# Optimization experiments

Hardware: AMD Instinct MI355X
Metric: run time of the kernel (lower is better)

## Reference

```python
import jax, jax.numpy as jnp
import numpy as np

M, K, N = 4096, 4096, 11008

def setup_inputs() -> dict:
    key = jax.random.key(0)
    k1, k2, k3, k4, k5 = jax.random.split(key, 5)
    x = jax.random.normal(k1, (M, K), dtype=jnp.float32)
    # int8 weights stored as int32 carrier (values in [-128, 127])
    weight = jax.random.randint(k2, (N, K), -128, 128, dtype=jnp.int32)
    # per-channel dequant scale, small positive values
    deq_scale = jax.random.uniform(k3, (N,), dtype=jnp.float32, minval=1e-4, maxval=2e-3)
    # static per-tensor activation scale
    input_scale = jax.random.uniform(k4, (1,), dtype=jnp.float32, minval=0.02, maxval=0.05)
    input_offset = jnp.zeros((1,), dtype=jnp.int32)
    quant_bias = jax.random.randint(k5, (N,), -1000, 1000, dtype=jnp.int32)
    return {"x": x, "weight": weight, "deq_scale": deq_scale,
            "input_scale": input_scale, "input_offset": input_offset,
            "quant_bias": quant_bias}

def reference(x, weight, deq_scale, input_scale, input_offset, quant_bias):
    # Static per-tensor activation quantization to int8
    x_q = jnp.clip(jnp.round(x / input_scale) + input_offset.astype(jnp.float32),
                   -128.0, 127.0).astype(jnp.int32)  # [M, K]
    # int8 GEMM accumulated in int32 (weight stored [N, K], i.e. transposed)
    acc = jnp.einsum('mk,nk->mn', x_q, weight)  # [M, N] int32
    # add int32 quant bias, per-channel dequant to fp32
    out = (acc + quant_bias[None, :]).astype(jnp.float32) * deq_scale[None, :]
    return out
```

## Files before the change

kernel.cpp:

```cpp
#include <hip/hip_runtime.h>
#include <cstdint>
#include <cstddef>

#define M_DIM 4096
#define K_DIM 4096
#define N_DIM 11008
#define BM 256
#define BN 256
#define BKB 128
#define NT (K_DIM / BKB)
#define NITER (NT / 2)
#define NTM (M_DIM / BM)
#define NTN (N_DIM / BN)
#define SLOT_BYTES 65536
#define B_OFF 32768

typedef int   int4v   __attribute__((ext_vector_type(4)));
typedef float float4v __attribute__((ext_vector_type(4)));

__device__ __forceinline__ void gload_lds16(const void* g, void* l) {
  __builtin_amdgcn_global_load_lds(
      (const __attribute__((address_space(1))) unsigned int*)g,
      (__attribute__((address_space(3))) unsigned int*)l, 16, 0, 0);
}

__global__ void quant_x_kernel(const float* __restrict__ x,
                               const float* __restrict__ scale_p,
                               const int* __restrict__ off_p,
                               signed char* __restrict__ xq, int total16) {
  const float inv = 1.0f / scale_p[0];
  const float off = (float)off_p[0];
  int tid = blockIdx.x * blockDim.x + threadIdx.x;
  int stride = gridDim.x * blockDim.x;
  const float4v* x4 = (const float4v*)x;
  int4v* out4 = (int4v*)xq;
  for (int i = tid; i < total16; i += stride) {
    int4v o;
#pragma unroll
    for (int j = 0; j < 4; ++j) {
      float4v v = x4[(size_t)i * 4 + j];
      int r = 0;
#pragma unroll
      for (int e = 0; e < 4; ++e) {
        float q = rintf(v[e] * inv) + off;
        q = fminf(fmaxf(q, -128.0f), 127.0f);
        int qi = (int)q;
        r |= (qi & 0xff) << (8 * e);
      }
      o[j] = r;
    }
    out4[i] = o;
  }
}

__global__ void pack_w_kernel(const int* __restrict__ w,
                              signed char* __restrict__ wq, int total16) {
  int tid = blockIdx.x * blockDim.x + threadIdx.x;
  int stride = gridDim.x * blockDim.x;
  const int4v* w4 = (const int4v*)w;
  int4v* out4 = (int4v*)wq;
  for (int i = tid; i < total16; i += stride) {
    int4v o;
#pragma unroll
    for (int j = 0; j < 4; ++j) {
      int4v v = w4[(size_t)i * 4 + j];
      o[j] = (v[0] & 0xff) | ((v[1] & 0xff) << 8) |
             ((v[2] & 0xff) << 16) | ((v[3] & 0xff) << 24);
    }
    out4[i] = o;
  }
}

__global__ __launch_bounds__(512, 2) void gemm_i8_kernel(
    const signed char* __restrict__ A,
    const signed char* __restrict__ B,
    const int* __restrict__ qbias,
    const float* __restrict__ dscale,
    float* __restrict__ out) {
  __shared__ __attribute__((aligned(16))) signed char lds[2 * SLOT_BYTES];

  const int tid  = threadIdx.x;
  const int lane = tid & 63;
  const int wv   = tid >> 6;
  const int wr   = wv >> 2;
  const int wc   = wv & 3;

  int bid = blockIdx.x;
  int swz = (bid & 7) * 86 + (bid >> 3);
  int tm = swz / NTN;
  int tn = swz % NTN;

  const int sks = wv & 1;
  const int r2  = wv >> 1;
  const int ro  = (r2 & 1) | ((r2 & 2) << 2);

  const signed char* pA = A + (size_t)(tm * BM + ro * 16 + (lane & 15)) * K_DIM
                            + sks * 64 + (lane >> 4) * 16;
  const signed char* pB = B + (size_t)(tn * BN + ro * 16 + (lane & 15)) * K_DIM
                            + sks * 64 + (lane >> 4) * 16;
  const int ldsA0 = (ro * 2 + sks) * 1024;
  const int ldsB0 = B_OFF + (ro * 2 + sks) * 1024;

#define STG(ktS, c) do {                                                      \
    int ktw_ = (ktS) & (NT - 1);                                              \
    int sl_  = (ktw_ & 1) * SLOT_BYTES;                                       \
    gload_lds16(pA + (size_t)(c) * 32 * K_DIM + (size_t)ktw_ * BKB,           \
                lds + sl_ + ldsA0 + (c) * 4096);                              \
    gload_lds16(pB + (size_t)(c) * 32 * K_DIM + (size_t)ktw_ * BKB,           \
                lds + sl_ + ldsB0 + (c) * 4096); } while (0)

  const int rdA0 = (wr * 8) * 2048 + lane * 16;
  const int rdB0 = B_OFF + (wc * 4) * 2048 + lane * 16;

  int4v acc[8][4];
#pragma unroll
  for (int i = 0; i < 8; ++i)
#pragma unroll
    for (int j = 0; j < 4; ++j) acc[i][j] = (int4v){0, 0, 0, 0};

  int4v bfr[4][2], afr[2][2];

#define PHASE(S, P, KTS, CH) do {                                             \
    const int sb_ = (S) * SLOT_BYTES;                                         \
    if ((P) == 0) {                                                           \
      _Pragma("unroll") for (int ni = 0; ni < 4; ++ni)                        \
        _Pragma("unroll") for (int ks = 0; ks < 2; ++ks)                      \
          bfr[ni][ks] = *(const int4v*)(lds + sb_ + rdB0 + ni * 2048 + ks * 1024); \
    }                                                                         \
    _Pragma("unroll") for (int d = 0; d < 2; ++d)                             \
      _Pragma("unroll") for (int ks = 0; ks < 2; ++ks)                        \
        afr[d][ks] = *(const int4v*)(lds + sb_ + rdA0 + (2 * (P) + d) * 2048 + ks * 1024); \
    STG(KTS, CH);                                                             \
    __builtin_amdgcn_s_barrier();                                             \
    asm volatile("s_waitcnt lgkmcnt(0)" ::: "memory");                        \
    __builtin_amdgcn_s_setprio(1);                                            \
    _Pragma("unroll") for (int d = 0; d < 2; ++d)                             \
      _Pragma("unroll") for (int ni = 0; ni < 4; ++ni)                        \
        _Pragma("unroll") for (int ks = 0; ks < 2; ++ks)                      \
          acc[2 * (P) + d][ni] = __builtin_amdgcn_mfma_i32_16x16x64_i8(       \
              afr[d][ks], bfr[ni][ks], acc[2 * (P) + d][ni], 0, 0, 0);        \
    __builtin_amdgcn_s_setprio(0);                                            \
    if ((P) == 3) asm volatile("s_waitcnt vmcnt(6)" ::: "memory");            \
    __builtin_amdgcn_s_barrier();                                             \
  } while (0)

#pragma unroll
  for (int c = 0; c < 4; ++c) STG(0, c);
#pragma unroll
  for (int c = 0; c < 3; ++c) STG(1, c);
  asm volatile("s_waitcnt vmcnt(6)" ::: "memory");
  __builtin_amdgcn_s_barrier();

  for (int t = 0; t < NITER; ++t) {
    const int k0 = 2 * t;
    PHASE(0, 0, k0 + 1, 3);
    PHASE(0, 1, k0 + 2, 0);
    PHASE(0, 2, k0 + 2, 1);
    PHASE(0, 3, k0 + 2, 2);
    PHASE(1, 0, k0 + 2, 3);
    PHASE(1, 1, k0 + 3, 0);
    PHASE(1, 2, k0 + 3, 1);
    PHASE(1, 3, k0 + 3, 2);
  }
  asm volatile("s_waitcnt vmcnt(0)" ::: "memory");
#undef PHASE
#undef STG

  const int col = lane & 15;
  const int rb  = (lane >> 4) * 4;
  const int gm0 = tm * BM + wr * 128;
  const int gn0 = tn * BN + wc * 64;
#pragma unroll
  for (int ni = 0; ni < 4; ++ni) {
    int gn = gn0 + ni * 16 + col;
    float ds = dscale[gn];
    int qb = qbias[gn];
#pragma unroll
    for (int mi = 0; mi < 8; ++mi) {
      int gm = gm0 + mi * 16 + rb;
#pragma unroll
      for (int j = 0; j < 4; ++j)
        out[(size_t)(gm + j) * N_DIM + gn] = (float)(acc[mi][ni][j] + qb) * ds;
    }
  }
}

extern "C" void kernel_launch(void* const* d_in, const int* in_sizes, int n_in,
                              void* d_out, int out_size, void* d_ws, size_t ws_size,
                              hipStream_t stream) {
  const float* x      = (const float*)d_in[0];
  const int*   w      = (const int*)d_in[1];
  const float* dscale = (const float*)d_in[2];
  const float* iscale = (const float*)d_in[3];
  const int*   ioff   = (const int*)d_in[4];
  const int*   qbias  = (const int*)d_in[5];
  float* out = (float*)d_out;

  const size_t xq_bytes = (size_t)M_DIM * K_DIM;
  const size_t wq_bytes = (size_t)N_DIM * K_DIM;
  if (ws_size < xq_bytes + wq_bytes) return;

  signed char* xq = (signed char*)d_ws;
  signed char* wq = (signed char*)d_ws + xq_bytes;

  quant_x_kernel<<<2048, 256, 0, stream>>>(x, iscale, ioff, xq, M_DIM * K_DIM / 16);
  pack_w_kernel<<<2048, 256, 0, stream>>>(w, wq, N_DIM * K_DIM / 16);
  gemm_i8_kernel<<<NTM * NTN, 512, 0, stream>>>(xq, wq, qbias, dscale, out);
}
```

Baseline: 287.0 us.

## Double-buffer register fragments to overlap LDS reads with MFMA in int8 GEMM

Restructures the main loop so LDS fragment reads for the next quarter-tile (and the next k-tile's B fragments) are issued before the MFMAs of the current quarter, using ping-pong A/B register buffers and partial lgkmcnt waits. This removes the full lgkmcnt(0) stall before each MFMA group. It also reduces barriers from two per phase to one and changes the global prefetch depth and vmcnt placement. The cost is higher register pressure, which may spill under launch_bounds(512,2), and a trickier cross-slot synchronization that could race if the waits are miscounted.

```diff
diff --git a/kernel.cpp b/kernel.cpp
--- a/kernel.cpp
+++ b/kernel.cpp
@@ -112,58 +112,94 @@
   const int rdA0 = (wr * 8) * 2048 + lane * 16;
   const int rdB0 = B_OFF + (wc * 4) * 2048 + lane * 16;
 
-  int4v acc[8][4];
-#pragma unroll
-  for (int i = 0; i < 8; ++i)
-#pragma unroll
-    for (int j = 0; j < 4; ++j) acc[i][j] = (int4v){0, 0, 0, 0};
-
-  int4v bfr[4][2], afr[2][2];
-
-#define PHASE(S, P, KTS, CH) do {                                             \
-    const int sb_ = (S) * SLOT_BYTES;                                         \
-    if ((P) == 0) {                                                           \
-      _Pragma("unroll") for (int ni = 0; ni < 4; ++ni)                        \
-        _Pragma("unroll") for (int ks = 0; ks < 2; ++ks)                      \
-          bfr[ni][ks] = *(const int4v*)(lds + sb_ + rdB0 + ni * 2048 + ks * 1024); \
-    }                                                                         \
+#define RD_A(dst, SB, QQ) do {                                                \
     _Pragma("unroll") for (int d = 0; d < 2; ++d)                             \
       _Pragma("unroll") for (int ks = 0; ks < 2; ++ks)                        \
-        afr[d][ks] = *(const int4v*)(lds + sb_ + rdA0 + (2 * (P) + d) * 2048 + ks * 1024); \
-    STG(KTS, CH);                                                             \
-    __builtin_amdgcn_s_barrier();                                             \
-    asm volatile("s_waitcnt lgkmcnt(0)" ::: "memory");                        \
+        dst[d][ks] = *(const int4v*)(lds + (SB) + rdA0 + (2*(QQ)+d)*2048 + ks*1024); \
+  } while (0)
+#define RD_B2(dst, SB, NI0) do {                                              \
+    _Pragma("unroll") for (int ii = 0; ii < 2; ++ii)                          \
+      _Pragma("unroll") for (int ks = 0; ks < 2; ++ks)                        \
+        dst[(NI0)+ii][ks] = *(const int4v*)(lds + (SB) + rdB0 + ((NI0)+ii)*2048 + ks*1024); \
+  } while (0)
+#define MFMA_Q(af, bf, QQ) do {                                               \
     __builtin_amdgcn_s_setprio(1);                                            \
     _Pragma("unroll") for (int d = 0; d < 2; ++d)                             \
       _Pragma("unroll") for (int ni = 0; ni < 4; ++ni)                        \
         _Pragma("unroll") for (int ks = 0; ks < 2; ++ks)                      \
-          acc[2 * (P) + d][ni] = __builtin_amdgcn_mfma_i32_16x16x64_i8(       \
-              afr[d][ks], bfr[ni][ks], acc[2 * (P) + d][ni], 0, 0, 0);        \
+          acc[2*(QQ)+d][ni] = __builtin_amdgcn_mfma_i32_16x16x64_i8(          \
+              af[d][ks], bf[ni][ks], acc[2*(QQ)+d][ni], 0, 0, 0);             \
     __builtin_amdgcn_s_setprio(0);                                            \
-    if ((P) == 3) asm volatile("s_waitcnt vmcnt(6)" ::: "memory");            \
-    __builtin_amdgcn_s_barrier();                                             \
-  } while (0)
+  } while (0)
+#define WAIT_LGKM(n) do {                                                     \
+    asm volatile("s_waitcnt lgkmcnt(" #n ")" ::: "memory");                   \
+    __builtin_amdgcn_sched_barrier(0);                                        \
+  } while (0)
+
+  int4v acc[8][4];
+#pragma unroll
+  for (int i = 0; i < 8; ++i)
+#pragma unroll
+    for (int j = 0; j < 4; ++j) acc[i][j] = (int4v){0, 0, 0, 0};
+
+  int4v afr0[2][2], afr1[2][2], bfr0[4][2], bfr1[4][2];
 
 #pragma unroll
   for (int c = 0; c < 4; ++c) STG(0, c);
 #pragma unroll
-  for (int c = 0; c < 3; ++c) STG(1, c);
-  asm volatile("s_waitcnt vmcnt(6)" ::: "memory");
+  for (int c = 0; c < 4; ++c) STG(1, c);
+  asm volatile("s_waitcnt vmcnt(8)" ::: "memory");
   __builtin_amdgcn_s_barrier();
+  RD_A(afr0, 0, 0);
+  RD_B2(bfr0, 0, 0);
+  RD_B2(bfr0, 0, 2);
+  asm volatile("s_waitcnt lgkmcnt(0)" ::: "memory");
+  __builtin_amdgcn_sched_barrier(0);
+  __builtin_amdgcn_s_barrier();
+
+#define TILE4(S, BFC, BFN, KST) do {                                          \
+    const int SB_  = (S) * SLOT_BYTES;                                        \
+    const int SBn_ = (1 - (S)) * SLOT_BYTES;                                  \
+                                                                      \
+    RD_A(afr1, SB_, 1);                                                       \
+    STG((KST), 0);                                                            \
+    __builtin_amdgcn_s_barrier();                                             \
+    WAIT_LGKM(4);                                                             \
+    MFMA_Q(afr0, BFC, 0);                                                     \
+                                                                      \
+    RD_A(afr0, SB_, 2);                                                       \
+    STG((KST), 1);                                                            \
+    asm volatile("s_waitcnt vmcnt(4)" ::: "memory");     \
+    __builtin_amdgcn_s_barrier();                                             \
+    WAIT_LGKM(4);                                                             \
+    MFMA_Q(afr1, BFC, 1);                                                     \
+                                                                      \
+    RD_A(afr1, SB_, 3);                                                       \
+    RD_B2(BFN, SBn_, 0);                                                      \
+    STG((KST), 2);                                                            \
+    __builtin_amdgcn_s_barrier();                                             \
+    WAIT_LGKM(8);                                                             \
+    MFMA_Q(afr0, BFC, 2);                                                     \
+                                                                      \
+    RD_A(afr0, SBn_, 0);                                                      \
+    RD_B2(BFN, SBn_, 2);                                                      \
+    STG((KST), 3);                                                            \
+    __builtin_amdgcn_s_barrier();                                             \
+    WAIT_LGKM(8);                                                             \
+    MFMA_Q(afr1, BFC, 3);                                                     \
+  } while (0)
 
   for (int t = 0; t < NITER; ++t) {
     const int k0 = 2 * t;
-    PHASE(0, 0, k0 + 1, 3);
-    PHASE(0, 1, k0 + 2, 0);
-    PHASE(0, 2, k0 + 2, 1);
-    PHASE(0, 3, k0 + 2, 2);
-    PHASE(1, 0, k0 + 2, 3);
-    PHASE(1, 1, k0 + 3, 0);
-    PHASE(1, 2, k0 + 3, 1);
-    PHASE(1, 3, k0 + 3, 2);
-  }
-  asm volatile("s_waitcnt vmcnt(0)" ::: "memory");
-#undef PHASE
+    TILE4(0, bfr0, bfr1, k0 + 2);
+    TILE4(1, bfr1, bfr0, k0 + 3);
+  }
+  asm volatile("s_waitcnt vmcnt(0) lgkmcnt(0)" ::: "memory");
+#undef TILE4
+#undef WAIT_LGKM
+#undef MFMA_Q
+#undef RD_B2
+#undef RD_A
 #undef STG
 
   const int col = lane & 15;
```

After: 284.5 us. No clear change (-0.9%).

## Restructure int8 GEMM to 4 waves with 128x128 per-wave tiles and register double-buffering

Applied to the files above, without the earlier changes.

Changes the GEMM block from 8 waves (each holding a 128x64 output tile) to 4 waves that each own a 128x128 tile, so every LDS fragment read feeds more MFMAs. The main loop now double-buffers A/B fragments in registers across the two k-halves and issues the next tile's global-to-LDS loads after a single barrier per k-step. The fine-grained phase schedule is removed, and the block-to-tile swizzle changes. The larger accumulator footprint (64 int4 accumulators plus four 8-entry fragment buffers) raises register pressure and lowers waves per CU, which may cost latency hiding.

```diff
diff --git a/kernel.cpp b/kernel.cpp
--- a/kernel.cpp
+++ b/kernel.cpp
@@ -9,7 +9,6 @@
 #define BN 256
 #define BKB 128
 #define NT (K_DIM / BKB)
-#define NITER (NT / 2)
 #define NTM (M_DIM / BM)
 #define NTN (N_DIM / BN)
 #define SLOT_BYTES 65536
@@ -71,7 +70,7 @@
   }
 }
 
-__global__ __launch_bounds__(512, 2) void gemm_i8_kernel(
+__global__ __launch_bounds__(256, 1) void gemm_i8_kernel(
     const signed char* __restrict__ A,
     const signed char* __restrict__ B,
     const int* __restrict__ qbias,
@@ -82,105 +81,102 @@
   const int tid  = threadIdx.x;
   const int lane = tid & 63;
   const int wv   = tid >> 6;
-  const int wr   = wv >> 2;
-  const int wc   = wv & 3;
+  const int wr   = wv >> 1;
+  const int wc   = wv & 1;
 
   int bid = blockIdx.x;
-  int swz = (bid & 7) * 86 + (bid >> 3);
-  int tm = swz / NTN;
-  int tn = swz % NTN;
-
-  const int sks = wv & 1;
-  const int r2  = wv >> 1;
-  const int ro  = (r2 & 1) | ((r2 & 2) << 2);
-
-  const signed char* pA = A + (size_t)(tm * BM + ro * 16 + (lane & 15)) * K_DIM
-                            + sks * 64 + (lane >> 4) * 16;
-  const signed char* pB = B + (size_t)(tn * BN + ro * 16 + (lane & 15)) * K_DIM
-                            + sks * 64 + (lane >> 4) * 16;
-  const int ldsA0 = (ro * 2 + sks) * 1024;
-  const int ldsB0 = B_OFF + (ro * 2 + sks) * 1024;
-
-#define STG(ktS, c) do {                                                      \
-    int ktw_ = (ktS) & (NT - 1);                                              \
-    int sl_  = (ktw_ & 1) * SLOT_BYTES;                                       \
-    gload_lds16(pA + (size_t)(c) * 32 * K_DIM + (size_t)ktw_ * BKB,           \
-                lds + sl_ + ldsA0 + (c) * 4096);                              \
-    gload_lds16(pB + (size_t)(c) * 32 * K_DIM + (size_t)ktw_ * BKB,           \
-                lds + sl_ + ldsB0 + (c) * 4096); } while (0)
-
-  const int rdA0 = (wr * 8) * 2048 + lane * 16;
-  const int rdB0 = B_OFF + (wc * 4) * 2048 + lane * 16;
-
-  int4v acc[8][4];
+  int s   = bid >> 3;
+  int tm  = 2 * (bid & 7) + (s & 1);
+  int tn  = s >> 1;
+
+  const signed char* pA = A + (size_t)(tm * BM + wv * 64 + (lane & 15)) * K_DIM
+                            + (lane >> 4) * 16;
+  const signed char* pB = B + (size_t)(tn * BN + wv * 64 + (lane & 15)) * K_DIM
+                            + (lane >> 4) * 16;
+
+#define STG(kt, so) do {                                                      \
+    _Pragma("unroll") for (int c = 0; c < 4; ++c)                             \
+      _Pragma("unroll") for (int ks = 0; ks < 2; ++ks) {                      \
+        gload_lds16(pA + (size_t)c * 16 * K_DIM + (size_t)(kt) * BKB + ks * 64, \
+                    lds + (so) + ((((wv * 4 + c) * 2 + ks)) << 10));          \
+        gload_lds16(pB + (size_t)c * 16 * K_DIM + (size_t)(kt) * BKB + ks * 64, \
+                    lds + (so) + B_OFF + ((((wv * 4 + c) * 2 + ks)) << 10));  \
+      } } while (0)
+
+#define RD_A(buf, so, ks) do {                                                \
+    _Pragma("unroll") for (int m = 0; m < 8; ++m)                             \
+      buf[m] = *(const int4v*)(lds + (so) +                                   \
+                (((wr * 8 + m) * 2 + (ks)) << 10) + lane * 16); } while (0)
+#define RD_B(buf, so, ks) do {                                                \
+    _Pragma("unroll") for (int n = 0; n < 8; ++n)                             \
+      buf[n] = *(const int4v*)(lds + (so) + B_OFF +                           \
+                (((wc * 8 + n) * 2 + (ks)) << 10) + lane * 16); } while (0)
+#define MFMA_S(ab, bb) do {                                                   \
+    _Pragma("unroll") for (int m = 0; m < 8; ++m)                             \
+      _Pragma("unroll") for (int n = 0; n < 8; ++n)                           \
+        acc[m][n] = __builtin_amdgcn_mfma_i32_16x16x64_i8(                    \
+            ab[m], bb[n], acc[m][n], 0, 0, 0); } while (0)
+#define WAIT_LGKM(k) do {                                                     \
+    asm volatile("s_waitcnt lgkmcnt(" #k ")" ::: "memory");                   \
+    __builtin_amdgcn_sched_barrier(0); } while (0)
+
+  int4v acc[8][8];
 #pragma unroll
   for (int i = 0; i < 8; ++i)
 #pragma unroll
-    for (int j = 0; j < 4; ++j) acc[i][j] = (int4v){0, 0, 0, 0};
-
-  int4v bfr[4][2], afr[2][2];
-
-#define PHASE(S, P, KTS, CH) do {                                             \
-    const int sb_ = (S) * SLOT_BYTES;                                         \
-    if ((P) == 0) {                                                           \
-      _Pragma("unroll") for (int ni = 0; ni < 4; ++ni)                        \
-        _Pragma("unroll") for (int ks = 0; ks < 2; ++ks)                      \
-          bfr[ni][ks] = *(const int4v*)(lds + sb_ + rdB0 + ni * 2048 + ks * 1024); \
-    }                                                                         \
-    _Pragma("unroll") for (int d = 0; d < 2; ++d)                             \
-      _Pragma("unroll") for (int ks = 0; ks < 2; ++ks)                        \
-        afr[d][ks] = *(const int4v*)(lds + sb_ + rdA0 + (2 * (P) + d) * 2048 + ks * 1024); \
-    STG(KTS, CH);                                                             \
-    __builtin_amdgcn_s_barrier();                                             \
-    asm volatile("s_waitcnt lgkmcnt(0)" ::: "memory");                        \
-    __builtin_amdgcn_s_setprio(1);                                            \
-    _Pragma("unroll") for (int d = 0; d < 2; ++d)                             \
-      _Pragma("unroll") for (int ni = 0; ni < 4; ++ni)                        \
-        _Pragma("unroll") for (int ks = 0; ks < 2; ++ks)                      \
-          acc[2 * (P) + d][ni] = __builtin_amdgcn_mfma_i32_16x16x64_i8(       \
-              afr[d][ks], bfr[ni][ks], acc[2 * (P) + d][ni], 0, 0, 0);        \
-    __builtin_amdgcn_s_setprio(0);                                            \
-    if ((P) == 3) asm volatile("s_waitcnt vmcnt(6)" ::: "memory");            \
-    __builtin_amdgcn_s_barrier();                                             \
-  } while (0)
-
-#pragma unroll
-  for (int c = 0; c < 4; ++c) STG(0, c);
-#pragma unroll
-  for (int c = 0; c < 3; ++c) STG(1, c);
-  asm volatile("s_waitcnt vmcnt(6)" ::: "memory");
+    for (int j = 0; j < 8; ++j) acc[i][j] = (int4v){0, 0, 0, 0};
+
+  int4v A0[8], A1[8], B0[8], B1[8];
+
+  STG(0, 0);
+  STG(1, SLOT_BYTES);
+  asm volatile("s_waitcnt vmcnt(16)" ::: "memory");
   __builtin_amdgcn_s_barrier();
-
-  for (int t = 0; t < NITER; ++t) {
-    const int k0 = 2 * t;
-    PHASE(0, 0, k0 + 1, 3);
-    PHASE(0, 1, k0 + 2, 0);
-    PHASE(0, 2, k0 + 2, 1);
-    PHASE(0, 3, k0 + 2, 2);
-    PHASE(1, 0, k0 + 2, 3);
-    PHASE(1, 1, k0 + 3, 0);
-    PHASE(1, 2, k0 + 3, 1);
-    PHASE(1, 3, k0 + 3, 2);
-  }
-  asm volatile("s_waitcnt vmcnt(0)" ::: "memory");
-#undef PHASE
+  __builtin_amdgcn_sched_barrier(0);
+  RD_A(A0, 0, 0);
+  RD_B(B0, 0, 0);
+
+  for (int kt = 0; kt < NT; ++kt) {
+    const int cur = (kt & 1) * SLOT_BYTES;
+    const int nxt = cur ^ SLOT_BYTES;
+
+    RD_A(A1, cur, 1);
+    WAIT_LGKM(8);
+    RD_B(B1, cur, 1);
+    MFMA_S(A0, B0);
+    WAIT_LGKM(8);
+    asm volatile("s_waitcnt vmcnt(0)" ::: "memory");
+    WAIT_LGKM(0);
+    __builtin_amdgcn_s_barrier();
+    __builtin_amdgcn_sched_barrier(0);
+    if (kt + 2 < NT) STG(kt + 2, cur);
+    if (kt + 1 < NT) {
+      RD_A(A0, nxt, 0);
+      RD_B(B0, nxt, 0);
+    }
+    MFMA_S(A1, B1);
+  }
+#undef WAIT_LGKM
+#undef MFMA_S
+#undef RD_B
+#undef RD_A
 #undef STG
 
   const int col = lane & 15;
   const int rb  = (lane >> 4) * 4;
   const int gm0 = tm * BM + wr * 128;
-  const int gn0 = tn * BN + wc * 64;
-#pragma unroll
-  for (int ni = 0; ni < 4; ++ni) {
-    int gn = gn0 + ni * 16 + col;
+  const int gn0 = tn * BN + wc * 128;
+#pragma unroll
+  for (int n = 0; n < 8; ++n) {
+    int gn = gn0 + n * 16 + col;
     float ds = dscale[gn];
     int qb = qbias[gn];
 #pragma unroll
-    for (int mi = 0; mi < 8; ++mi) {
-      int gm = gm0 + mi * 16 + rb;
+    for (int m = 0; m < 8; ++m) {
+      int gm = gm0 + m * 16 + rb;
 #pragma unroll
       for (int j = 0; j < 4; ++j)
-        out[(size_t)(gm + j) * N_DIM + gn] = (float)(acc[mi][ni][j] + qb) * ds;
+        out[(size_t)(gm + j) * N_DIM + gn] = (float)(acc[m][n][j] + qb) * ds;
     }
   }
 }
@@ -205,5 +201,5 @@
 
   quant_x_kernel<<<2048, 256, 0, stream>>>(x, iscale, ioff, xq, M_DIM * K_DIM / 16);
   pack_w_kernel<<<2048, 256, 0, stream>>>(w, wq, N_DIM * K_DIM / 16);
-  gemm_i8_kernel<<<NTM * NTN, 512, 0, stream>>>(xq, wq, qbias, dscale, out);
-}
+  gemm_i8_kernel<<<NTM * NTN, 256, 0, stream>>>(xq, wq, qbias, dscale, out);
+}
```

Measured after the change: 365.1 us. +27.2%, slower.

## Use XOR-swizzled LDS layout for int8 GEMM tiles and remap block order

Applied to the files above, without the earlier changes.

Changes the global-to-LDS staging so each row of A and B is stored contiguously with an XOR column swizzle. Reads use matching swizzled offsets, which should cut LDS bank conflicts on fragment loads. It also changes the block-to-tile mapping so consecutive blocks share B tiles across pairs of M tiles, and restructures the main loop into four phases per K step with alternating A fragment buffers. Barrier and waitcnt placement are reworked, which risks ordering hazards or added synchronisation cost.

```diff
diff --git a/kernel.cpp b/kernel.cpp
--- a/kernel.cpp
+++ b/kernel.cpp
@@ -9,7 +9,6 @@
 #define BN 256
 #define BKB 128
 #define NT (K_DIM / BKB)
-#define NITER (NT / 2)
 #define NTM (M_DIM / BM)
 #define NTN (N_DIM / BN)
 #define SLOT_BYTES 65536
@@ -86,85 +85,99 @@
   const int wc   = wv & 3;
 
   int bid = blockIdx.x;
-  int swz = (bid & 7) * 86 + (bid >> 3);
-  int tm = swz / NTN;
-  int tn = swz % NTN;
-
-  const int sks = wv & 1;
-  const int r2  = wv >> 1;
-  const int ro  = (r2 & 1) | ((r2 & 2) << 2);
-
-  const signed char* pA = A + (size_t)(tm * BM + ro * 16 + (lane & 15)) * K_DIM
-                            + sks * 64 + (lane >> 4) * 16;
-  const signed char* pB = B + (size_t)(tn * BN + ro * 16 + (lane & 15)) * K_DIM
-                            + sks * 64 + (lane >> 4) * 16;
-  const int ldsA0 = (ro * 2 + sks) * 1024;
-  const int ldsB0 = B_OFF + (ro * 2 + sks) * 1024;
-
-#define STG(ktS, c) do {                                                      \
-    int ktw_ = (ktS) & (NT - 1);                                              \
-    int sl_  = (ktw_ & 1) * SLOT_BYTES;                                       \
-    gload_lds16(pA + (size_t)(c) * 32 * K_DIM + (size_t)ktw_ * BKB,           \
-                lds + sl_ + ldsA0 + (c) * 4096);                              \
-    gload_lds16(pB + (size_t)(c) * 32 * K_DIM + (size_t)ktw_ * BKB,           \
-                lds + sl_ + ldsB0 + (c) * 4096); } while (0)
-
-  const int rdA0 = (wr * 8) * 2048 + lane * 16;
-  const int rdB0 = B_OFF + (wc * 4) * 2048 + lane * 16;
-
-  int4v acc[8][4];
-#pragma unroll
-  for (int i = 0; i < 8; ++i)
-#pragma unroll
-    for (int j = 0; j < 4; ++j) acc[i][j] = (int4v){0, 0, 0, 0};
-
-  int4v bfr[4][2], afr[2][2];
-
-#define PHASE(S, P, KTS, CH) do {                                             \
-    const int sb_ = (S) * SLOT_BYTES;                                         \
-    if ((P) == 0) {                                                           \
-      _Pragma("unroll") for (int ni = 0; ni < 4; ++ni)                        \
-        _Pragma("unroll") for (int ks = 0; ks < 2; ++ks)                      \
-          bfr[ni][ks] = *(const int4v*)(lds + sb_ + rdB0 + ni * 2048 + ks * 1024); \
-    }                                                                         \
-    _Pragma("unroll") for (int d = 0; d < 2; ++d)                             \
-      _Pragma("unroll") for (int ks = 0; ks < 2; ++ks)                        \
-        afr[d][ks] = *(const int4v*)(lds + sb_ + rdA0 + (2 * (P) + d) * 2048 + ks * 1024); \
-    STG(KTS, CH);                                                             \
-    __builtin_amdgcn_s_barrier();                                             \
-    asm volatile("s_waitcnt lgkmcnt(0)" ::: "memory");                        \
+  int s   = bid >> 3;
+  int tm  = 2 * (bid & 7) + (s & 1);
+  int tn  = s >> 1;
+
+  const int csw  = (((tid & 7) ^ ((tid >> 3) & 7)) << 4);
+  const int rA   = ((tid >> 8) << 7) + ((tid & 255) >> 3);
+  const signed char* sAp = A + (size_t)(tm * BM + rA) * K_DIM + csw;
+  const int dA0  = ((tid >> 8) << 14) + (((tid >> 6) & 3) << 10) + ((tid & 63) << 4);
+  const int rB   = tid >> 3;
+  const signed char* sBp = B + (size_t)(tn * BN + rB) * K_DIM + csw;
+  const int dB0  = B_OFF + (tid << 4);
+
+#define STGP(STEP, X) do {                                                    \
+    int st_ = (STEP) & (NT - 1);                                              \
+    int sl_ = (st_ & 1) * SLOT_BYTES;                                         \
+    gload_lds16(sAp + (size_t)(X) * 32 * K_DIM + (size_t)st_ * BKB,           \
+                lds + sl_ + dA0 + (X) * 4096);                                \
+    gload_lds16(sBp + (size_t)(X) * 64 * K_DIM + (size_t)st_ * BKB,           \
+                lds + sl_ + dB0 + (X) * 8192); } while (0)
+
+  const int sx  = (lane & 7) << 4;
+  const int q16 = ((lane >> 4) & 3) << 4;
+  const int ck0 = q16 ^ sx;
+  const int ck1 = (64 + q16) ^ sx;
+  const int rbA = (wr * 128 + (lane & 15)) * 128;
+  const int rbB = B_OFF + (wc * 64 + (lane & 15)) * 128;
+
+#define RDA(buf, SB, P) do {                                                  \
+    _Pragma("unroll") for (int d = 0; d < 2; ++d) {                           \
+      buf[d][0] = *(const int4v*)(lds + (SB) + rbA + (2*(P)+d)*2048 + ck0);   \
+      buf[d][1] = *(const int4v*)(lds + (SB) + rbA + (2*(P)+d)*2048 + ck1);   \
+    } } while (0)
+#define RDB(SB) do {                                                          \
+    _Pragma("unroll") for (int ni = 0; ni < 4; ++ni) {                        \
+      bfr[ni][0] = *(const int4v*)(lds + (SB) + rbB + ni*2048 + ck0);         \
+      bfr[ni][1] = *(const int4v*)(lds + (SB) + rbB + ni*2048 + ck1);         \
+    } } while (0)
+#define MM(af, P) do {                                                        \
     __builtin_amdgcn_s_setprio(1);                                            \
     _Pragma("unroll") for (int d = 0; d < 2; ++d)                             \
       _Pragma("unroll") for (int ni = 0; ni < 4; ++ni)                        \
         _Pragma("unroll") for (int ks = 0; ks < 2; ++ks)                      \
-          acc[2 * (P) + d][ni] = __builtin_amdgcn_mfma_i32_16x16x64_i8(       \
-              afr[d][ks], bfr[ni][ks], acc[2 * (P) + d][ni], 0, 0, 0);        \
-    __builtin_amdgcn_s_setprio(0);                                            \
-    if ((P) == 3) asm volatile("s_waitcnt vmcnt(6)" ::: "memory");            \
-    __builtin_amdgcn_s_barrier();                                             \
-  } while (0)
-
-#pragma unroll
-  for (int c = 0; c < 4; ++c) STG(0, c);
-#pragma unroll
-  for (int c = 0; c < 3; ++c) STG(1, c);
+          acc[2*(P)+d][ni] = __builtin_amdgcn_mfma_i32_16x16x64_i8(           \
+              af[d][ks], bfr[ni][ks], acc[2*(P)+d][ni], 0, 0, 0);             \
+    __builtin_amdgcn_s_setprio(0); } while (0)
+
+  int4v acc[8][4];
+#pragma unroll
+  for (int i = 0; i < 8; ++i)
+#pragma unroll
+    for (int j = 0; j < 4; ++j) acc[i][j] = (int4v){0, 0, 0, 0};
+
+  int4v af0[2][2], af1[2][2], bfr[4][2];
+
+  STGP(0, 0); STGP(0, 1); STGP(0, 2); STGP(0, 3);
+  STGP(1, 0); STGP(1, 1); STGP(1, 2);
   asm volatile("s_waitcnt vmcnt(6)" ::: "memory");
   __builtin_amdgcn_s_barrier();
 
-  for (int t = 0; t < NITER; ++t) {
-    const int k0 = 2 * t;
-    PHASE(0, 0, k0 + 1, 3);
-    PHASE(0, 1, k0 + 2, 0);
-    PHASE(0, 2, k0 + 2, 1);
-    PHASE(0, 3, k0 + 2, 2);
-    PHASE(1, 0, k0 + 2, 3);
-    PHASE(1, 1, k0 + 3, 0);
-    PHASE(1, 2, k0 + 3, 1);
-    PHASE(1, 3, k0 + 3, 2);
-  }
-  asm volatile("s_waitcnt vmcnt(0)" ::: "memory");
-#undef PHASE
-#undef STG
+  for (int t = 0; t < NT; ++t) {
+    const int sb = (t & 1) * SLOT_BYTES;
+    RDB(sb); RDA(af0, sb, 0);
+    STGP(t + 1, 3);
+    asm volatile("s_waitcnt lgkmcnt(8)" ::: "memory");
+    __builtin_amdgcn_s_barrier();
+    asm volatile("s_waitcnt lgkmcnt(0)" ::: "memory");
+    MM(af0, 0);
+    __builtin_amdgcn_s_barrier();
+    RDA(af1, sb, 1);
+    STGP(t + 2, 0);
+    __builtin_amdgcn_s_barrier();
+    asm volatile("s_waitcnt lgkmcnt(0)" ::: "memory");
+    MM(af1, 1);
+    __builtin_amdgcn_s_barrier();
+    RDA(af0, sb, 2);
+    STGP(t + 2, 1);
+    __builtin_amdgcn_s_barrier();
+    asm volatile("s_waitcnt lgkmcnt(0)" ::: "memory");
+    MM(af0, 2);
+    __builtin_amdgcn_s_barrier();
+    RDA(af1, sb, 3);
+    STGP(t + 2, 2);
+    __builtin_amdgcn_s_barrier();
+    asm volatile("s_waitcnt lgkmcnt(0)" ::: "memory");
+    MM(af1, 3);
+    asm volatile("s_waitcnt vmcnt(6)" ::: "memory");
+    __builtin_amdgcn_s_barrier();
+  }
+  asm volatile("s_waitcnt vmcnt(0) lgkmcnt(0)" ::: "memory");
+#undef MM
+#undef RDB
+#undef RDA
+#undef STGP
 
   const int col = lane & 15;
   const int rb  = (lane >> 4) * 4;
```

Result: faster. 252.8 us (-11.9%).
